# Performance work log

Hardware: AMD Instinct MI355X
Metric: run time of the kernel (lower is better)

Reference implementation:

```python
import jax, jax.numpy as jnp
import numpy as np

NIPSIN = [0, 1, 2]
MAXNIPSIN = max(NIPSIN)
MAXNUMTYPE = 4
NWAVE = 8
CUTOFF = 5.0
NUMATOM = 20000
NEDGE = 500000
HIDDEN = 128

_index_para = np.concatenate([np.full(3 ** i, j, dtype=np.int64) for j, i in enumerate(NIPSIN)])
P_ORI = int(_index_para.shape[0])  # 13 for nipsin=[0,1,2]
IPSIN = len(NIPSIN)
ONEHOT = jnp.asarray(np.eye(IPSIN, dtype=np.float32)[_index_para])  # [P_ORI, IPSIN]
INDEX_PARA = jnp.asarray(_index_para)
DFEAT = IPSIN * NWAVE


def _angular(dist_vec):
    # faithful to GetDensity.angular: concat of tensor-product powers of dist_vec
    n = dist_vec.shape[0]
    parts = [jnp.ones((n, 1), dist_vec.dtype), dist_vec]
    orbital = dist_vec
    num = 2
    for ip in range(1, MAXNIPSIN):
        orbital = jnp.einsum('ij,ik->ijk', orbital, dist_vec).reshape(n, -1)
        if ip + 1 == NIPSIN[num]:
            parts.append(orbital)
            num += 1
    return jnp.concatenate(parts, axis=1)  # [n, P_ORI]


def setup_inputs() -> dict:
    key = jax.random.key(0)
    ks = jax.random.split(key, 12)
    cart = jax.random.normal(ks[0], (NUMATOM, 3), dtype=jnp.float32) * 4.0
    neigh_list = jax.random.randint(ks[1], (2, NEDGE), 0, NUMATOM)
    shifts = jnp.zeros((NEDGE, 3), dtype=jnp.float32)
    species = jax.random.randint(ks[2], (NUMATOM,), 0, MAXNUMTYPE)
    rs = jax.random.uniform(ks[3], (MAXNUMTYPE, NWAVE), dtype=jnp.float32) * CUTOFF
    inta = jax.random.uniform(ks[4], (MAXNUMTYPE, NWAVE), dtype=jnp.float32) * 1.5 + 0.2
    params = 2.0 * jax.random.normal(ks[5], (MAXNUMTYPE, NWAVE), dtype=jnp.float32) - 1.0
    s1 = 1.0 / np.sqrt(DFEAT)
    s2 = 1.0 / np.sqrt(HIDDEN)
    return {
        'cart': cart, 'neigh_list': neigh_list, 'shifts': shifts, 'species': species,
        'rs': rs, 'inta': inta, 'params': params,
        'w1_0': jax.random.normal(ks[6], (DFEAT, HIDDEN), dtype=jnp.float32) * s1,
        'b1_0': jnp.zeros((HIDDEN,), dtype=jnp.float32),
        'w2_0': jax.random.normal(ks[7], (HIDDEN, DFEAT), dtype=jnp.float32) * s2,
        'b2_0': jnp.zeros((DFEAT,), dtype=jnp.float32),
        'w1_1': jax.random.normal(ks[8], (DFEAT, HIDDEN), dtype=jnp.float32) * s1,
        'b1_1': jnp.zeros((HIDDEN,), dtype=jnp.float32),
        'w2_1': jax.random.normal(ks[9], (HIDDEN, DFEAT), dtype=jnp.float32) * s2,
        'b2_1': jnp.zeros((DFEAT,), dtype=jnp.float32),
    }


def reference(cart, neigh_list, shifts, species, rs, inta, params,
              w1_0, b1_0, w2_0, b2_0, w1_1, b1_1, w2_1, b2_1):
    center = neigh_list[0]
    neigh = neigh_list[1]
    dist_vec = cart[center] - cart[neigh] - shifts            # [E,3]
    distances = jnp.linalg.norm(dist_vec, axis=-1)            # [E]
    fc = jnp.square(0.5 * jnp.cos(distances * (np.pi / CUTOFF)) + 0.5)
    ns = species[neigh]                                       # [E]
    # vectorized per-type gaussian (same math as the masked type loop)
    gauss = jnp.exp(-inta[ns] * jnp.square(distances[:, None] - rs[ns])) * params[ns]  # [E,NWAVE]
    ang = _angular(dist_vec)                                  # [E,P_ORI]
    radial = ang[:, :, None] * fc[:, None, None] * gauss[:, None, :]  # [E,P_ORI,NWAVE]
    orbital = jax.ops.segment_sum(radial, center, num_segments=NUMATOM)  # [A,P_ORI,NWAVE]
    density = jnp.einsum('apw,pi->aiw', jnp.square(orbital), ONEHOT).reshape(NUMATOM, -1)
    for (w1, b1, w2, b2) in ((w1_0, b1_0, w2_0, b2_0), (w1_1, b1_1, w2_1, b2_1)):
        output = jnp.tanh(density @ w1 + b1) @ w2 + b2        # [A,IPSIN*NWAVE]
        expand = output[neigh].reshape(-1, IPSIN, NWAVE)[:, INDEX_PARA, :]  # [E,P_ORI,NWAVE]
        sum_w = jax.ops.segment_sum(expand * radial, center, num_segments=NUMATOM)
        density = jnp.einsum('apw,pi->aiw', jnp.square(sum_w), ONEHOT).reshape(NUMATOM, -1)
    return density
```

## Files before the change

### kernel.cpp

```cpp
#include <hip/hip_runtime.h>
#include <math.h>

#define NATOM_FEAT 24
#define PORI 13
#define NW 8
#define CAP 64
#define CH 32
#define ANG_S 13
#define OG_S 26
#define WSLICE (CH * (ANG_S + OG_S))
#define HID 128

#define WAVE_SYNC() do { asm volatile("s_waitcnt lgkmcnt(0)" ::: "memory"); \
                         __builtin_amdgcn_wave_barrier(); } while (0)

__global__ void zero_k(int* __restrict__ p, int n)
{
    int i = blockIdx.x * blockDim.x + threadIdx.x;
    if (i < n) p[i] = 0;
}

__global__ void fill_k(const int* __restrict__ nl,
                       int* __restrict__ cursor,
                       const float* __restrict__ cart,
                       const float* __restrict__ shifts,
                       const int* __restrict__ species,
                       float4* __restrict__ slots,
                       int E)
{
    int e = blockIdx.x * blockDim.x + threadIdx.x;
    if (e >= E) return;
    int c = nl[e];
    int n = nl[E + e];
    float dx = cart[3*c+0] - cart[3*n+0] - shifts[3*e+0];
    float dy = cart[3*c+1] - cart[3*n+1] - shifts[3*e+1];
    float dz = cart[3*c+2] - cart[3*n+2] - shifts[3*e+2];
    int packed = n | (species[n] << 20);
    int ofs = atomicAdd(&cursor[c], 1);
    if (ofs < CAP)
        slots[(size_t)c * CAP + ofs] = make_float4(dx, dy, dz, __int_as_float(packed));
}

template<bool HASOUT, bool MLP>
__global__ __launch_bounds__(256, 8)
void atom_pass(const float4* __restrict__ slots,
               const int* __restrict__ cursor,
               const float* __restrict__ g_rs,
               const float* __restrict__ g_inta,
               const float* __restrict__ g_par,
               const float* __restrict__ outp_in,
               const float* __restrict__ w1, const float* __restrict__ b1,
               const float* __restrict__ w2, const float* __restrict__ b2,
               float* __restrict__ out,
               int A)
{
    __shared__ __align__(16) float smem[4 * WSLICE];
    int lane = threadIdx.x & 63;
    int wid  = threadIdx.x >> 6;
    float* ls = smem + wid * WSLICE;
    float* ls_ang = ls;
    float* ls_og  = ls + CH * ANG_S;
    float* orb_s = ls;
    float* dvec  = ls + 104;
    float* tvec  = ls + 128;

    int a = blockIdx.x * 4 + wid;
    if (a >= A) return;
    int cnt = min(cursor[a], CAP);

    int p  = lane >> 2, wq = lane & 3;
    int ip = (p == 0) ? 0 : ((p < 4) ? 1 : 2);
    int ogb = ip * NW + 2 * wq;

    float acc0 = 0.0f, acc1 = 0.0f;

    for (int s = 0; s < cnt; s += CH) {
        int m = min(CH, cnt - s);
        if (lane < m) {
            float4 D = slots[(size_t)a * CAP + s + lane];
            float ax = D.x, ay = D.y, az = D.z;
            int packed = __float_as_int(D.w);
            int n  = packed & 0xFFFFF;
            int sp = packed >> 20;

            float r  = sqrtf(ax*ax + ay*ay + az*az);
            float fcb = 0.5f * __cosf(r * 0.6283185307179586f) + 0.5f;
            float fc  = fcb * fcb;
            const float4* rs4 = (const float4*)(g_rs   + sp * NW);
            const float4* in4 = (const float4*)(g_inta + sp * NW);
            const float4* pa4 = (const float4*)(g_par  + sp * NW);
            float4 r0 = rs4[0], r1 = rs4[1];
            float4 i0 = in4[0], i1 = in4[1];
            float4 p0 = pa4[0], p1 = pa4[1];
            float go[NW];
            {
                const float* rr = (const float*)&r0;
                const float* ii = (const float*)&i0;
                const float* pp = (const float*)&p0;
                #pragma unroll
                for (int w = 0; w < 4; ++w) {
                    float dr = r - rr[w];
                    go[w] = __expf(-ii[w] * dr * dr) * pp[w] * fc;
                }
                const float* rr1 = (const float*)&r1;
                const float* ii1 = (const float*)&i1;
                const float* pp1 = (const float*)&p1;
                #pragma unroll
                for (int w = 0; w < 4; ++w) {
                    float dr = r - rr1[w];
                    go[w + 4] = __expf(-ii1[w] * dr * dr) * pp1[w] * fc;
                }
            }

            float* ar = ls_ang + lane * ANG_S;
            ar[0]  = 1.0f;
            ar[1]  = ax;    ar[2]  = ay;    ar[3]  = az;
            ar[4]  = ax*ax; ar[5]  = ax*ay; ar[6]  = ax*az;
            ar[7]  = ay*ax; ar[8]  = ay*ay; ar[9]  = ay*az;
            ar[10] = az*ax; ar[11] = az*ay; ar[12] = az*az;

            float2* ogr = (float2*)(ls_og + lane * OG_S);
            if (HASOUT) {
                const float4* orow = (const float4*)(outp_in + (size_t)n * NATOM_FEAT);
                float4 o0 = orow[0], o1 = orow[1], o2 = orow[2];
                float4 o3 = orow[3], o4 = orow[4], o5 = orow[5];
                const float* oa = (const float*)&o0;
                const float* ob = (const float*)&o1;
                const float* oc = (const float*)&o2;
                const float* od = (const float*)&o3;
                const float* oe = (const float*)&o4;
                const float* of = (const float*)&o5;
                #pragma unroll
                for (int q = 0; q < 4; ++q) {
                    ogr[q]     = make_float2(go[q]*oa[q], go[q+4]*ob[q]);
                    ogr[4 + q] = make_float2(go[q]*oc[q], go[q+4]*od[q]);
                    ogr[8 + q] = make_float2(go[q]*oe[q], go[q+4]*of[q]);
                }
            } else {
                #pragma unroll
                for (int q = 0; q < 4; ++q) {
                    float2 v = make_float2(go[q], go[q+4]);
                    ogr[q] = v; ogr[4 + q] = v; ogr[8 + q] = v;
                }
            }
        }
        WAVE_SYNC();
        if (lane < 52) {
            for (int j = 0; j < m; ++j) {
                float  av = ls_ang[j * ANG_S + p];
                float2 ov = *(const float2*)(ls_og + j * OG_S + ogb);
                acc0 += av * ov.x;
                acc1 += av * ov.y;
            }
        }
        WAVE_SYNC();
    }

    if (lane < 52) {
        orb_s[p * NW + wq]     = acc0 * acc0;
        orb_s[p * NW + wq + 4] = acc1 * acc1;
    }
    WAVE_SYNC();

    if (lane < NATOM_FEAT) {
        int i = lane >> 3, ww = lane & 7;
        float sum;
        if (i == 0) {
            sum = orb_s[ww];
        } else if (i == 1) {
            sum = orb_s[NW + ww] + orb_s[2*NW + ww] + orb_s[3*NW + ww];
        } else {
            sum = 0.0f;
            #pragma unroll
            for (int q = 4; q < PORI; ++q) sum += orb_s[q*NW + ww];
        }
        if (MLP) dvec[lane] = sum;
        else     out[(size_t)a * NATOM_FEAT + lane] = sum;
    }

    if (MLP) {
        WAVE_SYNC();
        float h0 = b1[lane], h1 = b1[lane + 64];
        #pragma unroll
        for (int j = 0; j < NATOM_FEAT; ++j) {
            float d = dvec[j];
            h0 += d * w1[j * HID + lane];
            h1 += d * w1[j * HID + lane + 64];
        }
        float e0 = __expf(2.0f * h0), e1 = __expf(2.0f * h1);
        tvec[lane]      = 1.0f - 2.0f / (e0 + 1.0f);
        tvec[lane + 64] = 1.0f - 2.0f / (e1 + 1.0f);
        WAVE_SYNC();
        int j  = (lane < 24) ? lane : lane - 24;
        int hb = (lane < 24) ? 0 : 64;
        float part = 0.0f;
        if (lane < 48) {
            #pragma unroll 8
            for (int h = 0; h < 64; ++h)
                part += tvec[hb + h] * w2[(hb + h) * NATOM_FEAT + j];
        }
        float other = __shfl(part, lane + 24);
        if (lane < NATOM_FEAT)
            out[(size_t)a * NATOM_FEAT + lane] = b2[lane] + part + other;
    }
}

extern "C" void kernel_launch(void* const* d_in, const int* in_sizes, int n_in,
                              void* d_out, int out_size, void* d_ws, size_t ws_size,
                              hipStream_t stream)
{
    const float* cart    = (const float*)d_in[0];
    const int*   nl      = (const int*)d_in[1];
    const float* shifts  = (const float*)d_in[2];
    const int*   species = (const int*)d_in[3];
    const float* rs      = (const float*)d_in[4];
    const float* inta    = (const float*)d_in[5];
    const float* params  = (const float*)d_in[6];
    const float* w1_0 = (const float*)d_in[7];
    const float* b1_0 = (const float*)d_in[8];
    const float* w2_0 = (const float*)d_in[9];
    const float* b2_0 = (const float*)d_in[10];
    const float* w1_1 = (const float*)d_in[11];
    const float* b1_1 = (const float*)d_in[12];
    const float* w2_1 = (const float*)d_in[13];
    const float* b2_1 = (const float*)d_in[14];

    const int A = in_sizes[0] / 3;
    const int E = in_sizes[1] / 2;

    char* ws = (char*)d_ws;
    float4* slots = (float4*)ws;              ws += (size_t)A * CAP * 16;
    int*   cursor = (int*)ws;                 ws += (size_t)A * 4;
    float* outpA  = (float*)ws;               ws += (size_t)A * NATOM_FEAT * 4;
    float* outpB  = (float*)ws;               ws += (size_t)A * NATOM_FEAT * 4;
    float* dout   = (float*)d_out;

    const int BLK = 256;
    const int gridE = (E + BLK - 1) / BLK;
    const int gridA = (A + BLK - 1) / BLK;
    const int gridP = (A + 3) / 4;

    zero_k<<<gridA, BLK, 0, stream>>>(cursor, A);
    fill_k<<<gridE, BLK, 0, stream>>>(nl, cursor, cart, shifts, species, slots, E);

    atom_pass<false, true><<<gridP, 256, 0, stream>>>(slots, cursor, rs, inta, params,
                                                      nullptr, w1_0, b1_0, w2_0, b2_0, outpA, A);
    atom_pass<true, true><<<gridP, 256, 0, stream>>>(slots, cursor, rs, inta, params,
                                                     outpA, w1_1, b1_1, w2_1, b2_1, outpB, A);
    atom_pass<true, false><<<gridP, 256, 0, stream>>>(slots, cursor, rs, inta, params,
                                                      outpB, nullptr, nullptr, nullptr, nullptr, dout, A);
}
```

Measured before the change: 120.9 us.

## Replace scatter fill with two-level partitioned binning of edges by center atom

The single fill kernel, which scattered each edge to a random center slot with global atomics, is replaced by a coarse partition pass followed by a per-partition slotting pass. The partition pass bins 2048-edge chunks into 16 center-atom ranges using shared-memory histograms, so the later scatter hits a localized, cache-resident region. It also packs cart and species into float4 to cut gather loads, and packs center, neighbor and species into one 32-bit word. This adds extra kernel launches and an intermediate buffer, and the 15-bit index packing and fixed partition capacity assume at most 32768 atoms and bounded partition sizes. The cutoff cosine also switches from __cosf to cosf.

```diff
diff --git a/kernel.cpp b/kernel.cpp
--- a/kernel.cpp
+++ b/kernel.cpp
@@ -11,6 +11,14 @@
 #define WSLICE (CH * (ANG_S + OG_S))
 #define HID 128
 
+#define NPART 16
+#define PSH 11
+#define PCAP 53248
+#define PA_T 256
+#define PA_E 8
+#define RECS (PA_T * PA_E)
+#define BPP 16
+
 #define WAVE_SYNC() do { asm volatile("s_waitcnt lgkmcnt(0)" ::: "memory"); \
                          __builtin_amdgcn_wave_barrier(); } while (0)
 
@@ -20,25 +28,99 @@
     if (i < n) p[i] = 0;
 }
 
-__global__ void fill_k(const int* __restrict__ nl,
-                       int* __restrict__ cursor,
-                       const float* __restrict__ cart,
-                       const float* __restrict__ shifts,
-                       const int* __restrict__ species,
-                       float4* __restrict__ slots,
-                       int E)
-{
-    int e = blockIdx.x * blockDim.x + threadIdx.x;
-    if (e >= E) return;
-    int c = nl[e];
-    int n = nl[E + e];
-    float dx = cart[3*c+0] - cart[3*n+0] - shifts[3*e+0];
-    float dy = cart[3*c+1] - cart[3*n+1] - shifts[3*e+1];
-    float dz = cart[3*c+2] - cart[3*n+2] - shifts[3*e+2];
-    int packed = n | (species[n] << 20);
-    int ofs = atomicAdd(&cursor[c], 1);
-    if (ofs < CAP)
-        slots[(size_t)c * CAP + ofs] = make_float4(dx, dy, dz, __int_as_float(packed));
+__global__ void cart4_k(const float* __restrict__ cart, const int* __restrict__ species,
+                        float4* __restrict__ cart4, int A)
+{
+    int i = blockIdx.x * blockDim.x + threadIdx.x;
+    if (i < A)
+        cart4[i] = make_float4(cart[3*i], cart[3*i+1], cart[3*i+2],
+                               __int_as_float(species[i]));
+}
+
+__global__ __launch_bounds__(PA_T)
+void part_k(const int* __restrict__ nl,
+            const float4* __restrict__ cart4,
+            const float* __restrict__ shifts,
+            int* __restrict__ pcur,
+            float4* __restrict__ bin,
+            int E)
+{
+    __shared__ float4 lrec[RECS];
+    __shared__ int histo[NPART], pstart[NPART + 1], cur[NPART], gbase[NPART];
+    int tid = threadIdx.x;
+    if (tid < NPART) histo[tid] = 0;
+    __syncthreads();
+
+    int e0 = blockIdx.x * RECS;
+    float4 rec[PA_E];
+    int pp[PA_E];
+    #pragma unroll
+    for (int k = 0; k < PA_E; ++k) {
+        int e = e0 + k * PA_T + tid;
+        pp[k] = -1;
+        if (e < E) {
+            int c = nl[e];
+            int n = nl[E + e];
+            float4 cc = cart4[c];
+            float4 cn = cart4[n];
+            float dx = cc.x - cn.x - shifts[3*e+0];
+            float dy = cc.y - cn.y - shifts[3*e+1];
+            float dz = cc.z - cn.z - shifts[3*e+2];
+            int sp = __float_as_int(cn.w);
+            int bits = n | (c << 15) | (sp << 30);
+            rec[k] = make_float4(dx, dy, dz, __int_as_float(bits));
+            pp[k]  = c >> PSH;
+            atomicAdd(&histo[pp[k]], 1);
+        }
+    }
+    __syncthreads();
+    if (tid == 0) {
+        int run = 0;
+        #pragma unroll
+        for (int i = 0; i < NPART; ++i) { pstart[i] = run; run += histo[i]; }
+        pstart[NPART] = run;
+    }
+    __syncthreads();
+    if (tid < NPART) {
+        gbase[tid] = histo[tid] ? atomicAdd(&pcur[tid * 16], histo[tid]) : 0;
+        cur[tid]   = pstart[tid];
+    }
+    __syncthreads();
+    #pragma unroll
+    for (int k = 0; k < PA_E; ++k) {
+        if (pp[k] >= 0) {
+            int s = atomicAdd(&cur[pp[k]], 1);
+            lrec[s] = rec[k];
+        }
+    }
+    __syncthreads();
+    int total = pstart[NPART];
+    for (int i = tid; i < total; i += PA_T) {
+        int p = 0;
+        while (pstart[p + 1] <= i) ++p;
+        int dst = gbase[p] + (i - pstart[p]);
+        if (dst < PCAP) bin[(size_t)p * PCAP + dst] = lrec[i];
+    }
+}
+
+__global__ __launch_bounds__(256)
+void slot2_k(const float4* __restrict__ bin,
+             const int* __restrict__ pcur,
+             float4* __restrict__ slots,
+             int* __restrict__ cursor,
+             int A)
+{
+    int p   = blockIdx.x / BPP;
+    int sub = blockIdx.x % BPP;
+    int cnt = min(pcur[p * 16], PCAP);
+    for (int i = sub * 256 + threadIdx.x; i < cnt; i += BPP * 256) {
+        float4 rec = bin[(size_t)p * PCAP + i];
+        int bits = __float_as_int(rec.w);
+        int c = (bits >> 15) & 0x7FFF;
+        int rank = atomicAdd(&cursor[c], 1);
+        if (rank < CAP)
+            slots[(size_t)c * CAP + rank] = rec;
+    }
 }
 
 template<bool HASOUT, bool MLP>
@@ -79,12 +161,12 @@
         if (lane < m) {
             float4 D = slots[(size_t)a * CAP + s + lane];
             float ax = D.x, ay = D.y, az = D.z;
-            int packed = __float_as_int(D.w);
-            int n  = packed & 0xFFFFF;
-            int sp = packed >> 20;
+            int bits = __float_as_int(D.w);
+            int n  = bits & 0x7FFF;
+            int sp = (bits >> 30) & 3;
 
             float r  = sqrtf(ax*ax + ay*ay + az*az);
-            float fcb = 0.5f * __cosf(r * 0.6283185307179586f) + 0.5f;
+            float fcb = 0.5f * cosf(r * 0.6283185307179586f) + 0.5f;
             float fc  = fcb * fcb;
             const float4* rs4 = (const float4*)(g_rs   + sp * NW);
             const float4* in4 = (const float4*)(g_inta + sp * NW);
@@ -96,19 +178,19 @@
             {
                 const float* rr = (const float*)&r0;
                 const float* ii = (const float*)&i0;
-                const float* pp = (const float*)&p0;
+                const float* pq = (const float*)&p0;
                 #pragma unroll
                 for (int w = 0; w < 4; ++w) {
                     float dr = r - rr[w];
-                    go[w] = __expf(-ii[w] * dr * dr) * pp[w] * fc;
+                    go[w] = __expf(-ii[w] * dr * dr) * pq[w] * fc;
                 }
                 const float* rr1 = (const float*)&r1;
                 const float* ii1 = (const float*)&i1;
-                const float* pp1 = (const float*)&p1;
+                const float* pq1 = (const float*)&p1;
                 #pragma unroll
                 for (int w = 0; w < 4; ++w) {
                     float dr = r - rr1[w];
-                    go[w + 4] = __expf(-ii1[w] * dr * dr) * pp1[w] * fc;
+                    go[w + 4] = __expf(-ii1[w] * dr * dr) * pq1[w] * fc;
                 }
             }
 
@@ -230,18 +312,23 @@
 
     char* ws = (char*)d_ws;
     float4* slots = (float4*)ws;              ws += (size_t)A * CAP * 16;
+    float4* bin   = (float4*)ws;              ws += (size_t)NPART * PCAP * 16;
+    float4* cart4 = (float4*)ws;              ws += (size_t)A * 16;
     int*   cursor = (int*)ws;                 ws += (size_t)A * 4;
+    int*   pcur   = (int*)ws;                 ws += (size_t)NPART * 16 * 4;
     float* outpA  = (float*)ws;               ws += (size_t)A * NATOM_FEAT * 4;
     float* outpB  = (float*)ws;               ws += (size_t)A * NATOM_FEAT * 4;
     float* dout   = (float*)d_out;
 
     const int BLK = 256;
-    const int gridE = (E + BLK - 1) / BLK;
     const int gridA = (A + BLK - 1) / BLK;
     const int gridP = (A + 3) / 4;
-
-    zero_k<<<gridA, BLK, 0, stream>>>(cursor, A);
-    fill_k<<<gridE, BLK, 0, stream>>>(nl, cursor, cart, shifts, species, slots, E);
+    const int gridPart = (E + RECS - 1) / RECS;
+
+    zero_k<<<(A + NPART * 16 + BLK - 1) / BLK, BLK, 0, stream>>>(cursor, A + NPART * 16);
+    cart4_k<<<gridA, BLK, 0, stream>>>(cart, species, cart4, A);
+    part_k<<<gridPart, PA_T, 0, stream>>>(nl, cart4, shifts, pcur, bin, E);
+    slot2_k<<<NPART * BPP, 256, 0, stream>>>(bin, pcur, slots, cursor, A);
 
     atom_pass<false, true><<<gridP, 256, 0, stream>>>(slots, cursor, rs, inta, params,
                                                       nullptr, w1_0, b1_0, w2_0, b2_0, outpA, A);
```

New measurement: 134.8 us. 1.11x slower.
